# Kernel tuning notes

Hardware: AMD Instinct MI355X
Metric: run time of the kernel (lower is better)

Reference implementation:

```python
import jax, jax.numpy as jnp
import numpy as np

B, S, D = 4, 2048, 1024
H = 16
HD = D // H  # 64
FF = 4096


def setup_inputs() -> dict:
    key = jax.random.key(0)
    ks = jax.random.split(key, 11)
    sd = 1.0 / np.sqrt(D)
    inp = {
        "embeddings": jax.random.normal(ks[0], (B, S, D), dtype=jnp.float32),
        # per-head Linear weights stacked: [H, head_dim, D] (torch Linear layout)
        "Wq": jax.random.uniform(ks[1], (H, HD, D), jnp.float32, -sd, sd),
        "bq": jax.random.uniform(ks[2], (H, HD), jnp.float32, -sd, sd),
        "Wk": jax.random.uniform(ks[3], (H, HD, D), jnp.float32, -sd, sd),
        "bk": jax.random.uniform(ks[4], (H, HD), jnp.float32, -sd, sd),
        "Wv": jax.random.uniform(ks[5], (H, HD, D), jnp.float32, -sd, sd),
        "bv": jax.random.uniform(ks[6], (H, HD), jnp.float32, -sd, sd),
        "W1": jax.random.uniform(ks[7], (FF, D), jnp.float32, -sd, sd),
        "b1": jax.random.uniform(ks[8], (FF,), jnp.float32, -sd, sd),
        "W2": jax.random.uniform(ks[9], (D, FF), jnp.float32, -1.0 / np.sqrt(FF), 1.0 / np.sqrt(FF)),
        "b2": jax.random.uniform(ks[10], (D,), jnp.float32, -1.0 / np.sqrt(FF), 1.0 / np.sqrt(FF)),
    }
    return inp


def reference(embeddings, Wq, bq, Wk, bk, Wv, bv, W1, b1, W2, b2):
    # Per-head projections, batched over heads: [B,H,S,HD]
    Q = jnp.einsum("bsd,hed->bhse", embeddings, Wq) + bq[None, :, None, :]
    K = jnp.einsum("bsd,hed->bhse", embeddings, Wk) + bk[None, :, None, :]
    V = jnp.einsum("bsd,hed->bhse", embeddings, Wv) + bv[None, :, None, :]
    # NOTE: original scales by sqrt(embed_dim), not sqrt(head_dim)
    scale = 1.0 / jnp.sqrt(jnp.asarray(D, embeddings.dtype))
    scores = jnp.einsum("bhse,bhte->bhst", Q, K) * scale  # [B,H,S,S]
    A = jax.nn.softmax(scores, axis=-1)
    Hh = jnp.einsum("bhst,bhte->bhse", A, V)  # [B,H,S,HD]
    # concat heads along last dim (head order matches torch.cat)
    Hcat = jnp.transpose(Hh, (0, 2, 1, 3)).reshape(B, S, D)
    hid = jax.nn.relu(Hcat @ W1.T + b1)
    return hid @ W2.T + b2
```

## Files before the change

### kernel.cpp

```cpp
#include <hip/hip_runtime.h>
#include <stdint.h>


typedef __attribute__((ext_vector_type(8))) short bf16x8;
typedef __attribute__((ext_vector_type(4))) float f32x4;

__device__ __forceinline__ float bf2f(unsigned short u) {
  union { float f; uint32_t i; } v; v.i = ((uint32_t)u) << 16; return v.f;
}
__device__ __forceinline__ unsigned short f2bf(float f) {
  union { float f; uint32_t i; } v; v.f = f;
  uint32_t i = v.i;
  return (unsigned short)((i + 0x7fffu + ((i >> 16) & 1u)) >> 16);
}

#if __has_builtin(__builtin_amdgcn_exp2f)
#define EXP2(x) __builtin_amdgcn_exp2f(x)
#else
#define EXP2(x) __expf((x) * 0.6931471805599453f)
#endif

__device__ __forceinline__ uint32_t pk_bf16(float p0, float p1) {
  union { float f; uint32_t i; } a, b; a.f = p0; b.f = p1;
  return __builtin_amdgcn_perm(b.i + 0x8000u, a.i + 0x8000u, 0x07060302u);
}

__device__ __forceinline__ void gld16(const void* g, void* l) {
  __builtin_amdgcn_global_load_lds(
      (const __attribute__((address_space(1))) uint32_t*)(uintptr_t)g,
      (__attribute__((address_space(3))) uint32_t*)(uintptr_t)l, 16, 0, 0);
}

#define SCALE_Q 0.04508422002778011f

#define W1B          0
#define W2B    4194304
#define B1B    8388608
#define B2B    8392704
#define BQB    8393728
#define BKB    8394752
#define BVB    8395776
#define EMBB   8396800
#define WQB   16785408
#define WKB   17833984
#define WVB   18882560
#define QOFF  19931136
#define KOFF  28319744
#define VTOFF 36708352
#define HCOFF 45096960
#define HIDOFF 8396800

__global__ void cvt_all(const float* __restrict__ emb, const float* __restrict__ Wq,
                        const float* __restrict__ bq,  const float* __restrict__ Wk,
                        const float* __restrict__ bk,  const float* __restrict__ Wv,
                        const float* __restrict__ bv,  const float* __restrict__ W1,
                        const float* __restrict__ b1,  const float* __restrict__ W2,
                        const float* __restrict__ b2,  unsigned short* __restrict__ ws) {
  const int i4 = blockIdx.x * 256 + threadIdx.x;
  if (i4 >= 4982784) return;
  const float* s; unsigned short* d; int base;
  if      (i4 < 2097152) { s = emb; d = ws + EMBB; base = 0; }
  else if (i4 < 2359296) { s = Wq;  d = ws + WQB;  base = 2097152; }
  else if (i4 < 2621440) { s = Wk;  d = ws + WKB;  base = 2359296; }
  else if (i4 < 2883584) { s = Wv;  d = ws + WVB;  base = 2621440; }
  else if (i4 < 3932160) { s = W1;  d = ws + W1B;  base = 2883584; }
  else if (i4 < 4980736) { s = W2;  d = ws + W2B;  base = 3932160; }
  else if (i4 < 4980992) { s = bq;  d = ws + BQB;  base = 4980736; }
  else if (i4 < 4981248) { s = bk;  d = ws + BKB;  base = 4980992; }
  else if (i4 < 4981504) { s = bv;  d = ws + BVB;  base = 4981248; }
  else if (i4 < 4982528) { s = b1;  d = ws + B1B;  base = 4981504; }
  else                   { s = b2;  d = ws + B2B;  base = 4982528; }
  const int j = i4 - base;
  const float4 v = ((const float4*)s)[j];
  ushort4 o;
  o.x = f2bf(v.x); o.y = f2bf(v.y); o.z = f2bf(v.z); o.w = f2bf(v.w);
  *(ushort4*)(d + (size_t)j * 4) = o;
}

template <int MODE>
__launch_bounds__(256, 2)
__global__ void gemm128(const unsigned short* __restrict__ A,
                        const unsigned short* __restrict__ W0,
                        const unsigned short* __restrict__ W1p,
                        const unsigned short* __restrict__ W2p,
                        const unsigned short* __restrict__ bias0,
                        const unsigned short* __restrict__ bias1,
                        const unsigned short* __restrict__ bias2,
                        unsigned short* __restrict__ out0,
                        unsigned short* __restrict__ out1,
                        unsigned short* __restrict__ out2,
                        float* __restrict__ foutp,
                        int N, int K) {
  __shared__ unsigned short At[128 * 32];
  __shared__ unsigned short Bt[128 * 32];
  const int tid  = threadIdx.x;
  const int wave = tid >> 6, lane = tid & 63;
  const int quad = lane >> 4, l15 = lane & 15;
  const int rowBase = blockIdx.y * 128;
  const int colBase = blockIdx.x * 128;

  const unsigned short* W = W0;
  const unsigned short* bias = bias0;
  int colW = colBase;
  if (MODE == 2) {
    const int which = colBase >> 10;
    if (which == 1) { W = W1p; bias = bias1; }
    if (which == 2) { W = W2p; bias = bias2; }
    colW = colBase & 1023;
  }

  const int u0 = tid, u1 = tid + 256;
  const int r0 = u0 >> 2, e0 = (((u0 & 3) ^ ((r0 >> 2) & 3)) * 8);
  const int r1 = u1 >> 2, e1 = (((u1 & 3) ^ ((r1 >> 2) & 3)) * 8);
  const unsigned short* gA0 = A + (size_t)(rowBase + r0) * K + e0;
  const unsigned short* gA1 = A + (size_t)(rowBase + r1) * K + e1;
  const unsigned short* gB0 = W + (size_t)(colW + r0) * K + e0;
  const unsigned short* gB1 = W + (size_t)(colW + r1) * K + e1;
  unsigned short* lA0 = At + u0 * 8;
  unsigned short* lA1 = At + u1 * 8;
  unsigned short* lB0 = Bt + u0 * 8;
  unsigned short* lB1 = Bt + u1 * 8;

  const int wrow = (wave & 1) * 64, wcol = (wave >> 1) * 64;
  int aoff[4], boff[4];
#pragma unroll
  for (int t = 0; t < 4; ++t) {
    const int ra = wrow + t * 16 + l15;
    aoff[t] = ra * 32 + ((quad ^ ((ra >> 2) & 3)) * 8);
    const int rb = wcol + t * 16 + l15;
    boff[t] = rb * 32 + ((quad ^ ((rb >> 2) & 3)) * 8);
  }

  f32x4 acc[4][4] = {};
  for (int k0 = 0; k0 < K; k0 += 32) {
    __syncthreads();
    gld16(gA0, lA0); gld16(gA1, lA1);
    gld16(gB0, lB0); gld16(gB1, lB1);
    gA0 += 32; gA1 += 32; gB0 += 32; gB1 += 32;
    __syncthreads();
    bf16x8 af[4], bfr[4];
#pragma unroll
    for (int t = 0; t < 4; ++t) af[t]  = *(const bf16x8*)(At + aoff[t]);
#pragma unroll
    for (int t = 0; t < 4; ++t) bfr[t] = *(const bf16x8*)(Bt + boff[t]);
#pragma unroll
    for (int mt = 0; mt < 4; ++mt)
#pragma unroll
      for (int nt = 0; nt < 4; ++nt)
        acc[mt][nt] = __builtin_amdgcn_mfma_f32_16x16x32_bf16(
            af[mt], bfr[nt], acc[mt][nt], 0, 0, 0);
  }

#pragma unroll
  for (int mt = 0; mt < 4; ++mt) {
    const int row = rowBase + wrow + mt * 16 + quad * 4;
#pragma unroll
    for (int nt = 0; nt < 4; ++nt) {
      const int cIn = colW + wcol + nt * 16 + l15;
      const float bv = bf2f(bias[cIn]);
      if (MODE == 2) {
        const int which = colBase >> 10;
        const int h = cIn >> 6, e = cIn & 63;
#pragma unroll
        for (int r = 0; r < 4; ++r) {
          const int tok = row + r;
          const int b = tok >> 11, s = tok & 2047;
          const float v = acc[mt][nt][r] + bv;
          const size_t bh = (size_t)(b * 16 + h);
          if (which == 0)      out0[(bh * 2048 + s) * 64 + e] = f2bf(v * SCALE_Q);
          else if (which == 1) out1[(bh * 2048 + s) * 64 + e] = f2bf(v);
          else                 out2[(bh * 64 + e) * 2048 + s] = f2bf(v);
        }
      } else if (MODE == 1) {
#pragma unroll
        for (int r = 0; r < 4; ++r) {
          const float v = fmaxf(acc[mt][nt][r] + bv, 0.0f);
          out0[(size_t)(row + r) * N + cIn] = f2bf(v);
        }
      } else {
#pragma unroll
        for (int r = 0; r < 4; ++r)
          foutp[(size_t)(row + r) * N + cIn] = acc[mt][nt][r] + bv;
      }
    }
  }
}

__launch_bounds__(256, 4)
__global__ void flash_attn(const unsigned short* __restrict__ Q,
                           const unsigned short* __restrict__ Kg,
                           const unsigned short* __restrict__ Vt,
                           unsigned short* __restrict__ Hc) {
  __shared__ unsigned short Kt[64 * 64];
  __shared__ unsigned short Vs[64 * 64];
  __shared__ unsigned short Pl[4][32 * 64];
  __shared__ float Lb[4][32];
  const int tid  = threadIdx.x;
  const int wave = tid >> 6, lane = tid & 63;
  const int quad = lane >> 4, l15 = lane & 15;
  const int bh = blockIdx.y;
  const int q0 = blockIdx.x * 128 + wave * 32;
  const size_t base = (size_t)bh * (2048 * 64);
  const unsigned short* Qb = Q  + base;
  const unsigned short* Kb = Kg + base;
  const unsigned short* Vb = Vt + base;

  bf16x8 qf[2][2];
#pragma unroll
  for (int qt = 0; qt < 2; ++qt) {
    const int q = q0 + qt * 16 + l15;
#pragma unroll
    for (int kk = 0; kk < 2; ++kk)
      qf[qt][kk] = *(const bf16x8*)(Qb + (size_t)q * 64 + kk * 32 + quad * 8);
  }

  const int u0 = tid, u1 = tid + 256;
  const int kr0 = u0 >> 3, kc0 = (((u0 & 7) ^ (kr0 & 7)) * 8);
  const int kr1 = u1 >> 3, kc1 = (((u1 & 7) ^ (kr1 & 7)) * 8);
  const unsigned short* gK0 = Kb + (size_t)kr0 * 64 + kc0;
  const unsigned short* gK1 = Kb + (size_t)kr1 * 64 + kc1;
  const unsigned short* gV0 = Vb + (size_t)kr0 * 2048 + kc0;
  const unsigned short* gV1 = Vb + (size_t)kr1 * 2048 + kc1;
  unsigned short* lK0 = Kt + u0 * 8;
  unsigned short* lK1 = Kt + u1 * 8;
  unsigned short* lV0 = Vs + u0 * 8;
  unsigned short* lV1 = Vs + u1 * 8;

  float l_acc[2] = {0.0f, 0.0f};
  f32x4 o[2][4] = {};
  unsigned short* Pw = Pl[wave];

  for (int it = 0; it < 32; ++it) {
    __syncthreads();
    gld16(gK0, lK0); gld16(gK1, lK1);
    gld16(gV0, lV0); gld16(gV1, lV1);
    gK0 += 4096; gK1 += 4096; gV0 += 64; gV1 += 64;
    __syncthreads();

    f32x4 st[4][2] = {};
#pragma unroll
    for (int tt = 0; tt < 4; ++tt) {
      const int t = tt * 16 + l15;
      const bf16x8 kf0 = *(const bf16x8*)(Kt + t * 64 + ((quad       ^ (t & 7)) * 8));
      const bf16x8 kf1 = *(const bf16x8*)(Kt + t * 64 + (((quad + 4) ^ (t & 7)) * 8));
#pragma unroll
      for (int qt = 0; qt < 2; ++qt) {
        st[tt][qt] = __builtin_amdgcn_mfma_f32_16x16x32_bf16(kf0, qf[qt][0], st[tt][qt], 0, 0, 0);
        st[tt][qt] = __builtin_amdgcn_mfma_f32_16x16x32_bf16(kf1, qf[qt][1], st[tt][qt], 0, 0, 0);
      }
    }

#pragma unroll
    for (int tt = 0; tt < 4; ++tt) {
      const int tc = tt * 2 + (quad >> 1);
#pragma unroll
      for (int qt = 0; qt < 2; ++qt) {
        const float p0 = EXP2(st[tt][qt][0]);
        const float p1 = EXP2(st[tt][qt][1]);
        const float p2 = EXP2(st[tt][qt][2]);
        const float p3 = EXP2(st[tt][qt][3]);
        l_acc[qt] += (p0 + p1) + (p2 + p3);
        uint2 w;
        w.x = pk_bf16(p0, p1);
        w.y = pk_bf16(p2, p3);
        const int qrow = qt * 16 + l15;
        *(uint2*)(Pw + qrow * 64 + ((tc ^ (qrow & 7)) * 8) + (quad & 1) * 4) = w;
      }
    }

    bf16x8 pf[2][2];
#pragma unroll
    for (int mt = 0; mt < 2; ++mt) {
      const int qq = mt * 16 + l15;
      pf[mt][0] = *(const bf16x8*)(Pw + qq * 64 + ((quad       ^ (qq & 7)) * 8));
      pf[mt][1] = *(const bf16x8*)(Pw + qq * 64 + (((quad + 4) ^ (qq & 7)) * 8));
    }
#pragma unroll
    for (int nt = 0; nt < 4; ++nt) {
      const int e = nt * 16 + l15;
      const bf16x8 vf0 = *(const bf16x8*)(Vs + e * 64 + ((quad       ^ (e & 7)) * 8));
      const bf16x8 vf1 = *(const bf16x8*)(Vs + e * 64 + (((quad + 4) ^ (e & 7)) * 8));
#pragma unroll
      for (int mt = 0; mt < 2; ++mt) {
        o[mt][nt] = __builtin_amdgcn_mfma_f32_16x16x32_bf16(pf[mt][0], vf0, o[mt][nt], 0, 0, 0);
        o[mt][nt] = __builtin_amdgcn_mfma_f32_16x16x32_bf16(pf[mt][1], vf1, o[mt][nt], 0, 0, 0);
      }
    }
  }

#pragma unroll
  for (int qt = 0; qt < 2; ++qt) {
    float v = l_acc[qt];
    v += __shfl_xor(v, 16, 64);
    v += __shfl_xor(v, 32, 64);
    Lb[wave][qt * 16 + l15] = v;
  }
  const f32x4 lv0 = *(const f32x4*)&Lb[wave][quad * 4];
  const f32x4 lv1 = *(const f32x4*)&Lb[wave][16 + quad * 4];

  const int b = bh >> 4, h = bh & 15;
#pragma unroll
  for (int mt = 0; mt < 2; ++mt)
#pragma unroll
    for (int r = 0; r < 4; ++r) {
      const int qg = q0 + mt * 16 + quad * 4 + r;
      const float inv = __builtin_amdgcn_rcpf(mt == 0 ? lv0[r] : lv1[r]);
#pragma unroll
      for (int nt = 0; nt < 4; ++nt) {
        const int e = nt * 16 + l15;
        Hc[((size_t)b * 2048 + qg) * 1024 + h * 64 + e] = f2bf(o[mt][nt][r] * inv);
      }
    }
}

extern "C" void kernel_launch(void* const* d_in, const int* in_sizes, int n_in,
                              void* d_out, int out_size, void* d_ws, size_t ws_size,
                              hipStream_t stream) {
  const float* emb = (const float*)d_in[0];
  const float* Wq  = (const float*)d_in[1];
  const float* bq  = (const float*)d_in[2];
  const float* Wk  = (const float*)d_in[3];
  const float* bk  = (const float*)d_in[4];
  const float* Wv  = (const float*)d_in[5];
  const float* bv  = (const float*)d_in[6];
  const float* W1  = (const float*)d_in[7];
  const float* b1  = (const float*)d_in[8];
  const float* W2  = (const float*)d_in[9];
  const float* b2  = (const float*)d_in[10];

  unsigned short* ws = (unsigned short*)d_ws;
  float* out = (float*)d_out;

  cvt_all<<<19465, 256, 0, stream>>>(emb, Wq, bq, Wk, bk, Wv, bv, W1, b1, W2, b2, ws);
  gemm128<2><<<dim3(24, 64), 256, 0, stream>>>(
      ws + EMBB, ws + WQB, ws + WKB, ws + WVB, ws + BQB, ws + BKB, ws + BVB,
      ws + QOFF, ws + KOFF, ws + VTOFF, nullptr, 3072, 1024);
  flash_attn<<<dim3(16, 64), 256, 0, stream>>>(ws + QOFF, ws + KOFF, ws + VTOFF, ws + HCOFF);
  gemm128<1><<<dim3(32, 64), 256, 0, stream>>>(
      ws + HCOFF, ws + W1B, nullptr, nullptr, ws + B1B, nullptr, nullptr,
      ws + HIDOFF, nullptr, nullptr, nullptr, 4096, 1024);
  gemm128<0><<<dim3(8, 64), 256, 0, stream>>>(
      ws + HIDOFF, ws + W2B, nullptr, nullptr, ws + B2B, nullptr, nullptr,
      nullptr, nullptr, nullptr, out, 1024, 4096);
}
```

Baseline: 492.9 us.

## Remap block IDs for XCD locality and use fragment-ordered LDS tiles

Block indices in the GEMM and flash-attention kernels are remapped so that groups of eight consecutive launched blocks, which round-robin across the MI355X's XCDs, share the same column tile or the same head. This aims to improve L2 reuse per XCD. The GEMM's LDS staging layout is also reorganised so each 16-row fragment sits contiguously in lane order, replacing the XOR swizzle with direct lane*8 reads. The remap assumes grid sizes are multiples of 64 row tiles and 64 heads, and the new layout may change bank-conflict behaviour on the LDS writes.

Result: slower. 568.4 us (+15.3%).

```diff
diff --git a/kernel.cpp b/kernel.cpp
--- a/kernel.cpp
+++ b/kernel.cpp
@@ -96,8 +96,11 @@
   const int tid  = threadIdx.x;
   const int wave = tid >> 6, lane = tid & 63;
   const int quad = lane >> 4, l15 = lane & 15;
-  const int rowBase = blockIdx.y * 128;
-  const int colBase = blockIdx.x * 128;
+
+  const int lid = blockIdx.x + blockIdx.y * gridDim.x;
+  const int s_ = lid >> 3;
+  const int rowBase = (((lid & 7) + ((s_ & 7) << 3)) << 7);
+  const int colBase = ((s_ >> 3) << 7);
 
   const unsigned short* W = W0;
   const unsigned short* bias = bias0;
@@ -110,12 +113,12 @@
   }
 
   const int u0 = tid, u1 = tid + 256;
-  const int r0 = u0 >> 2, e0 = (((u0 & 3) ^ ((r0 >> 2) & 3)) * 8);
-  const int r1 = u1 >> 2, e1 = (((u1 & 3) ^ ((r1 >> 2) & 3)) * 8);
-  const unsigned short* gA0 = A + (size_t)(rowBase + r0) * K + e0;
-  const unsigned short* gA1 = A + (size_t)(rowBase + r1) * K + e1;
-  const unsigned short* gB0 = W + (size_t)(colW + r0) * K + e0;
-  const unsigned short* gB1 = W + (size_t)(colW + r1) * K + e1;
+  const int r0 = ((u0 >> 6) << 4) | (u0 & 15), c0 = (u0 >> 4) & 3;
+  const int r1 = ((u1 >> 6) << 4) | (u1 & 15), c1 = (u1 >> 4) & 3;
+  const unsigned short* gA0 = A + (size_t)(rowBase + r0) * K + c0 * 8;
+  const unsigned short* gA1 = A + (size_t)(rowBase + r1) * K + c1 * 8;
+  const unsigned short* gB0 = W + (size_t)(colW + r0) * K + c0 * 8;
+  const unsigned short* gB1 = W + (size_t)(colW + r1) * K + c1 * 8;
   unsigned short* lA0 = At + u0 * 8;
   unsigned short* lA1 = At + u1 * 8;
   unsigned short* lB0 = Bt + u0 * 8;
@@ -125,10 +128,8 @@
   int aoff[4], boff[4];
 #pragma unroll
   for (int t = 0; t < 4; ++t) {
-    const int ra = wrow + t * 16 + l15;
-    aoff[t] = ra * 32 + ((quad ^ ((ra >> 2) & 3)) * 8);
-    const int rb = wcol + t * 16 + l15;
-    boff[t] = rb * 32 + ((quad ^ ((rb >> 2) & 3)) * 8);
+    aoff[t] = ((wrow >> 4) + t) * 512 + lane * 8;
+    boff[t] = ((wcol >> 4) + t) * 512 + lane * 8;
   }
 
   f32x4 acc[4][4] = {};
@@ -198,8 +199,12 @@
   const int tid  = threadIdx.x;
   const int wave = tid >> 6, lane = tid & 63;
   const int quad = lane >> 4, l15 = lane & 15;
-  const int bh = blockIdx.y;
-  const int q0 = blockIdx.x * 128 + wave * 32;
+
+  const int lid = blockIdx.x + blockIdx.y * gridDim.x;
+  const int s_ = lid >> 3;
+  const int bh = (lid & 7) + ((s_ & 7) << 3);
+  const int q0 = ((s_ >> 3) << 7) + wave * 32;
+
   const size_t base = (size_t)bh * (2048 * 64);
   const unsigned short* Qb = Q  + base;
   const unsigned short* Kb = Kg + base;
```
